# Kernel optimization log

Measured on AMD Instinct MI355X. Metric: run time of the kernel, lower is better.

Reference implementation:

```python
import jax, jax.numpy as jnp
import numpy as np

EMBED = 128
HEADS = 8
HEAD_DIM = EMBED // HEADS
MARKOFF = -1.0e8


def setup_inputs() -> dict:
    key = jax.random.key(0)
    ks = jax.random.split(key, 10)
    B, N, T, E = 2, 512, 12, EMBED
    values = jax.random.normal(ks[0], (B, N, T, E), dtype=jnp.float32)
    keys = jax.random.normal(ks[1], (B, N, T, E), dtype=jnp.float32)
    query = jax.random.normal(ks[2], (B, N, T, E), dtype=jnp.float32)
    # binary spatial mask [N, N] (1 = attend, 0 = block), kept float as in the torch code
    mask = (jax.random.uniform(ks[3], (N, N)) > 0.1).astype(jnp.float32)
    # per-head projections (nn.Linear on last dim of size head_dim, no bias)
    s = 1.0 / np.sqrt(HEAD_DIM)
    Wv = jax.random.uniform(ks[4], (HEAD_DIM, HEAD_DIM), minval=-s, maxval=s, dtype=jnp.float32)
    Wk = jax.random.uniform(ks[5], (HEAD_DIM, HEAD_DIM), minval=-s, maxval=s, dtype=jnp.float32)
    Wq = jax.random.uniform(ks[6], (HEAD_DIM, HEAD_DIM), minval=-s, maxval=s, dtype=jnp.float32)
    so = 1.0 / np.sqrt(EMBED)
    Wo = jax.random.uniform(ks[7], (EMBED, EMBED), minval=-so, maxval=so, dtype=jnp.float32)
    bo = jax.random.uniform(ks[8], (EMBED,), minval=-so, maxval=so, dtype=jnp.float32)
    return {"values": values, "keys": keys, "query": query, "mask": mask,
            "Wv": Wv, "Wk": Wk, "Wq": Wq, "Wo": Wo, "bo": bo}


def reference(values, keys, query, mask, Wv, Wk, Wq, Wo, bo):
    B, N, T, E = query.shape
    H, D = HEADS, HEAD_DIM
    scale = E ** 0.5
    v = values.reshape(B, N, T, H, D) @ Wv.T   # [B,N,T,H,D]
    k = keys.reshape(B, N, T, H, D) @ Wk.T
    q = query.reshape(B, N, T, H, D) @ Wq.T
    # energy over node axis: [B, Nq, Nk, T, H]
    energy = jnp.einsum('bqthd,bkthd->bqkth', q, k)
    m = mask[None, :, :, None, None]
    energy = energy * m + MARKOFF * (1.0 - m)
    # NOTE: softmax over the QUERY axis (dim=1), as in the original
    attention = jax.nn.softmax(jnp.clip(energy / scale, -5.0, 5.0), axis=1)
    out = jnp.einsum('bqkth,bkthd->bqthd', attention, v).reshape(B, N, T, H * D)
    out = out @ Wo.T + bo
    return out, attention
```

## Files before the change

kernel.cpp:

```cpp
#include <hip/hip_runtime.h>
#include <math.h>

#define DI __device__ __forceinline__

typedef short s16x8 __attribute__((ext_vector_type(8)));
typedef float f32x4 __attribute__((ext_vector_type(4)));

constexpr float MARKOFF_ = -100000000.0f;
constexpr float INVSCALE_ = 0.088388347648318447f;

DI s16x8 bc(uint4 u) { return __builtin_bit_cast(s16x8, u); }
DI unsigned short f2bf(float f) {
  unsigned u = __float_as_uint(f);
  return (unsigned short)((u + 0x7FFFu + ((u >> 16) & 1u)) >> 16);
}
DI float bf2f(unsigned short h) { return __uint_as_float(((unsigned)h) << 16); }
DI unsigned cvtpk(float lo, float hi) {
  unsigned r;
  asm("v_cvt_pk_bf16_f32 %0, %1, %2" : "=v"(r) : "v"(lo), "v"(hi));
  return r;
}

DI void load16(float* dst, const float* src) {
  #pragma unroll
  for (int c = 0; c < 4; ++c) {
    float4 v = reinterpret_cast<const float4*>(src)[c];
    dst[c * 4 + 0] = v.x; dst[c * 4 + 1] = v.y;
    dst[c * 4 + 2] = v.z; dst[c * 4 + 3] = v.w;
  }
}

DI float dotw4(const float4* w4, const float* x) {
  float s = 0.f;
  #pragma unroll
  for (int c = 0; c < 4; ++c) {
    float4 w = w4[c];
    s = fmaf(w.x, x[4*c], fmaf(w.y, x[4*c+1], fmaf(w.z, x[4*c+2], fmaf(w.w, x[4*c+3], s))));
  }
  return s;
}

DI void packstore(ushort* dst, const float* y) {
  ushort hs[16];
  #pragma unroll
  for (int d = 0; d < 16; ++d) hs[d] = f2bf(y[d]);
  unsigned hi[8], lo[8];
  #pragma unroll
  for (int i = 0; i < 8; ++i) {
    hi[i] = (unsigned)hs[2*i] | ((unsigned)hs[2*i+1] << 16);
    float l0 = y[2*i]   - bf2f(hs[2*i]);
    float l1 = y[2*i+1] - bf2f(hs[2*i+1]);
    lo[i] = (unsigned)f2bf(l0) | ((unsigned)f2bf(l1) << 16);
  }
  uint4* p = (uint4*)dst;
  p[0] = make_uint4(hi[0], hi[1], hi[2], hi[3]);
  p[1] = make_uint4(hi[4], hi[5], hi[6], hi[7]);
  p[2] = make_uint4(lo[0], lo[1], lo[2], lo[3]);
  p[3] = make_uint4(lo[4], lo[5], lo[6], lo[7]);
}

__global__ __launch_bounds__(256) void k_proj(
    const float* __restrict__ vals, const float* __restrict__ keys,
    const float* __restrict__ qry, const float* __restrict__ Wv,
    const float* __restrict__ Wk, const float* __restrict__ Wq,
    ushort* __restrict__ Qp, ushort* __restrict__ Kp, ushort* __restrict__ Vt) {
  __shared__ float wlds[768];
  __shared__ ushort vtile[16 * 16 * 16];
  int blk = blockIdx.x;
  int nc = blk & 31, SL = blk >> 5;
  int b = SL / 6, t2 = SL % 6;
  int tid = threadIdx.x;
  if (tid < 256) {
    wlds[tid] = Wq[tid];
    wlds[256 + tid] = Wk[tid];
    wlds[512 + tid] = Wv[tid];
  }
  __syncthreads();
  int th = tid & 15, nl = tid >> 4;
  int t = 2 * t2 + (th >> 3), h = th & 7;
  int key = (th & 3) << 2;
  int n = nc * 16 + nl;
  size_t ioff = ((size_t)(b * 512 + n) * 12 + t) * 128 + h * 16;
  float xq[16], xk[16], xv[16], y[16];
  load16(xq, qry + ioff);
  load16(xk, keys + ioff);
  load16(xv, vals + ioff);
  size_t orow = ((size_t)(SL * 512 + n) * 16 + th) * 32;
  #pragma unroll
  for (int d = 0; d < 16; ++d) y[d] = dotw4((const float4*)&wlds[d * 16], xq);
  packstore(Qp + orow, y);
  #pragma unroll
  for (int d = 0; d < 16; ++d) y[d] = dotw4((const float4*)&wlds[256 + d * 16], xk);
  packstore(Kp + orow, y);
  #pragma unroll
  for (int d = 0; d < 16; ++d) y[d] = dotw4((const float4*)&wlds[512 + d * 16], xv);
  #pragma unroll
  for (int d = 0; d < 16; ++d) vtile[th * 256 + d * 16 + (nl ^ key)] = f2bf(y[d]);
  __syncthreads();
  #pragma unroll
  for (int it = 0; it < 2; ++it) {
    int u = tid + it * 256;
    int thd = u >> 1, half = u & 1;
    int thw = thd >> 4;
    uint4 v = *(const uint4*)&vtile[thd * 16 + half * 8];
    if (thw & 1) {
      unsigned t0 = v.x; v.x = v.z; v.z = t0;
      t0 = v.y; v.y = v.w; v.w = t0;
    }
    int lhalf = half ^ ((thw >> 1) & 1);
    *(uint4*)(Vt + (size_t)(SL * 256 + thd) * 512 + nc * 16 + lhalf * 8) = v;
  }
}

__global__ __launch_bounds__(256) void k_colsum(
    const ushort* __restrict__ Qp, const ushort* __restrict__ Kp,
    const float* __restrict__ mask, float* __restrict__ cs) {
  int blk = blockIdx.x;
  int qs = blk & 3, kc = (blk >> 2) & 15, SL = blk >> 6;
  int tid = threadIdx.x;
  int l = tid & 63, wv = tid >> 6, c = l & 15, g = l >> 4, thb = wv * 4;
  uint4 zz = make_uint4(0, 0, 0, 0);
  s16x8 Bk1[2][4], Bk2[2][4];
  #pragma unroll
  for (int e = 0; e < 2; ++e) {
    int kb = kc * 32 + e * 16;
    #pragma unroll
    for (int j = 0; j < 4; ++j) {
      const uint4* row = (const uint4*)(Kp + ((size_t)(SL * 512 + kb + c) * 16 + thb + j) * 32);
      Bk1[e][j] = bc(row[g & 1]);
      Bk2[e][j] = bc(g < 2 ? row[2 + (g & 1)] : zz);
    }
  }
  float sum[2][4] = {{0.f, 0.f, 0.f, 0.f}, {0.f, 0.f, 0.f, 0.f}};
  for (int qtl = 0; qtl < 8; ++qtl) {
    int qb = qs * 128 + qtl * 16;
    float m[2][4];
    #pragma unroll
    for (int e = 0; e < 2; ++e) {
      int kb = kc * 32 + e * 16;
      #pragma unroll
      for (int r = 0; r < 4; ++r)
        m[e][r] = mask[(size_t)(qb + 4 * g + r) * 512 + kb + c];
    }
    #pragma unroll
    for (int j = 0; j < 4; ++j) {
      const uint4* qrow = (const uint4*)(Qp + ((size_t)(SL * 512 + qb + c) * 16 + thb + j) * 32);
      s16x8 A1 = bc(qrow[g]);
      s16x8 A2 = bc(qrow[g & 1]);
      #pragma unroll
      for (int e = 0; e < 2; ++e) {
        f32x4 C = __builtin_amdgcn_mfma_f32_16x16x32_bf16(A1, Bk1[e][j], (f32x4){0.f,0.f,0.f,0.f}, 0, 0, 0);
        C = __builtin_amdgcn_mfma_f32_16x16x32_bf16(A2, Bk2[e][j], C, 0, 0, 0);
        #pragma unroll
        for (int r = 0; r < 4; ++r) {
          float Em = m[e][r] > 0.5f ? C[r] : MARKOFF_;
          float x = fminf(fmaxf(Em * INVSCALE_, -5.f), 5.f);
          sum[e][j] += __expf(x);
        }
      }
    }
  }
  #pragma unroll
  for (int e = 0; e < 2; ++e)
    #pragma unroll
    for (int j = 0; j < 4; ++j) {
      float s = sum[e][j];
      s += __shfl_xor(s, 16, 64);
      s += __shfl_xor(s, 32, 64);
      if (l < 16)
        cs[((size_t)(qs * 12 + SL) * 16 + thb + j) * 512 + kc * 32 + e * 16 + c] = s;
    }
}

__global__ __launch_bounds__(256) void k_inv(const float* __restrict__ cs,
                                             float* __restrict__ inv) {
  int id = blockIdx.x * 256 + threadIdx.x;
  float s = cs[id] + cs[id + 98304] + cs[id + 196608] + cs[id + 294912];
  inv[id] = 1.0f / s;
}

__global__ __launch_bounds__(256, 4) void k_attn(
    const ushort* __restrict__ Qp, const ushort* __restrict__ Kp,
    const ushort* __restrict__ Vt, const float* __restrict__ mask,
    const float* __restrict__ inv, float* __restrict__ Aout,
    float* __restrict__ Oh, int KS) {
  __shared__ __align__(16) float stage[5184];
  int blk = blockIdx.x;
  int ksp = blk & (KS - 1);
  int rest = blk / KS;
  int qt = rest & 31, SL = rest >> 5;
  int b = SL / 6, t2 = SL % 6;
  int qb = qt * 16;
  int tid = threadIdx.x;
  int l = tid & 63, wv = tid >> 6, c = l & 15, g = l >> 4, thb = wv * 4;
  uint4 zz = make_uint4(0, 0, 0, 0);
  s16x8 Bq1[4], Bq2[4];
  #pragma unroll
  for (int j = 0; j < 4; ++j) {
    const uint4* row = (const uint4*)(Qp + ((size_t)(SL * 512 + qb + c) * 16 + thb + j) * 32);
    Bq1[j] = bc(row[g & 1]);
    Bq2[j] = bc(g < 2 ? row[2 + (g & 1)] : zz);
  }
  f32x4 O[4];
  #pragma unroll
  for (int j = 0; j < 4; ++j) O[j] = (f32x4){0.f, 0.f, 0.f, 0.f};

  int nch = 16 / KS;
  for (int cc = 0; cc < nch; ++cc) {
    int kch = ksp * (512 / KS) + cc * 32;
    unsigned apk[4][4];
    #pragma unroll
    for (int h = 0; h < 2; ++h) {
      int kb = kch + h * 16;
      float4 m4 = *(const float4*)(mask + (size_t)(qb + c) * 512 + kb + 4 * g);
      float m[4] = {m4.x, m4.y, m4.z, m4.w};
      float p[4][4];
      #pragma unroll
      for (int j = 0; j < 4; ++j) {
        const uint4* krow = (const uint4*)(Kp + ((size_t)(SL * 512 + kb + c) * 16 + thb + j) * 32);
        s16x8 A1 = bc(krow[g]);
        s16x8 A2 = bc(krow[g & 1]);
        f32x4 C = __builtin_amdgcn_mfma_f32_16x16x32_bf16(A1, Bq1[j], (f32x4){0.f,0.f,0.f,0.f}, 0, 0, 0);
        C = __builtin_amdgcn_mfma_f32_16x16x32_bf16(A2, Bq2[j], C, 0, 0, 0);
        float4 i4 = *(const float4*)(inv + (size_t)(SL * 16 + thb + j) * 512 + kb + 4 * g);
        float iv[4] = {i4.x, i4.y, i4.z, i4.w};
        #pragma unroll
        for (int r = 0; r < 4; ++r) {
          float Em = m[r] > 0.5f ? C[r] : MARKOFF_;
          float x = fminf(fmaxf(Em * INVSCALE_, -5.f), 5.f);
          p[j][r] = __expf(x) * iv[r];
        }
        apk[j][h * 2 + 0] = cvtpk(p[j][0], p[j][1]);
        apk[j][h * 2 + 1] = cvtpk(p[j][2], p[j][3]);
      }
      #pragma unroll
      for (int r = 0; r < 4; ++r) {
        f32x4 w = {p[0][r], p[1][r], p[2][r], p[3][r]};
        *(f32x4*)&stage[(4 * g + r) * 324 + c * 20 + thb] = w;
      }
      if (h == 1) {
        #pragma unroll
        for (int j = 0; j < 4; ++j) {
          const ushort* vb = Vt + ((size_t)(SL * 16 + thb + j) * 16 + c) * 512 + kch + 4 * g;
          uint2 v0 = *(const uint2*)vb;
          uint2 v1 = *(const uint2*)(vb + 16);
          s16x8 a_op = bc(make_uint4(apk[j][0], apk[j][1], apk[j][2], apk[j][3]));
          s16x8 b_op = bc(make_uint4(v0.x, v0.y, v1.x, v1.y));
          O[j] = __builtin_amdgcn_mfma_f32_16x16x32_bf16(a_op, b_op, O[j], 0, 0, 0);
        }
      }
      __syncthreads();
      #pragma unroll
      for (int it = 0; it < 4; ++it) {
        int m5 = tid & 3, pr = tid >> 2;
        int kk = pr & 15, q = (pr >> 4) + it * 4;
        f32x4 v = *(const f32x4*)&stage[kk * 324 + q * 20 + m5 * 4];
        size_t ga = ((size_t)(b * 512 + qb + q) * 512 + kb + kk) * 96 + t2 * 16 + m5 * 4;
        __builtin_nontemporal_store(v, (f32x4*)(Aout + ga));
      }
      __syncthreads();
    }
  }
  #pragma unroll
  for (int j = 0; j < 4; ++j) {
    int th = thb + j, t = 2 * t2 + (th >> 3), h = th & 7;
    float* op = Oh + (size_t)ksp * 1572864;
    #pragma unroll
    for (int r = 0; r < 4; ++r)
      op[((size_t)(b * 512 + qb + 4 * g + r) * 12 + t) * 128 + h * 16 + c] = O[j][r];
  }
}

__global__ __launch_bounds__(128) void k_outproj(
    const float* __restrict__ Oh, const float* __restrict__ Wo,
    const float* __restrict__ bo, float* __restrict__ out, int KS) {
  __shared__ float xr[12 * 128];
  int bn = blockIdx.x;
  int b = bn >> 9, n = bn & 511;
  int col = threadIdx.x;
  for (int i = col; i < 1536; i += 128) {
    float s = 0.f;
    for (int sl = 0; sl < KS; ++sl)
      s += Oh[(size_t)sl * 1572864 + (size_t)(b * 512 + n) * 1536 + i];
    xr[i] = s;
  }
  __syncthreads();
  float acc[12];
  float bias = bo[col];
  #pragma unroll
  for (int rr = 0; rr < 12; ++rr) acc[rr] = bias;
  const float4* wrow = reinterpret_cast<const float4*>(Wo + (size_t)col * 128);
  #pragma unroll 8
  for (int jc = 0; jc < 32; ++jc) {
    float4 w = wrow[jc];
    #pragma unroll
    for (int rr = 0; rr < 12; ++rr) {
      const float* x = &xr[rr * 128 + jc * 4];
      acc[rr] = fmaf(w.x, x[0], fmaf(w.y, x[1], fmaf(w.z, x[2], fmaf(w.w, x[3], acc[rr]))));
    }
  }
  size_t obase = ((size_t)(b * 512 + n)) * 1536;
  #pragma unroll
  for (int rr = 0; rr < 12; ++rr) out[obase + rr * 128 + col] = acc[rr];
}

extern "C" void kernel_launch(void* const* d_in, const int* in_sizes, int n_in,
                              void* d_out, int out_size, void* d_ws, size_t ws_size,
                              hipStream_t stream) {
  (void)in_sizes; (void)n_in; (void)out_size;
  const float* vals = (const float*)d_in[0];
  const float* keys = (const float*)d_in[1];
  const float* qry  = (const float*)d_in[2];
  const float* mask = (const float*)d_in[3];
  const float* Wv = (const float*)d_in[4];
  const float* Wk = (const float*)d_in[5];
  const float* Wq = (const float*)d_in[6];
  const float* Wo = (const float*)d_in[7];
  const float* bo = (const float*)d_in[8];
  float* out = (float*)d_out;
  float* Aout = out + 1572864;

  ushort* Qp = (ushort*)d_ws;
  ushort* Kp = Qp + 3145728;
  ushort* Vt = Kp + 3145728;
  float* cs  = (float*)(Vt + 1572864);
  float* inv = cs + 393216;
  float* Oh  = inv + 98304;

  const size_t BASE = 17694720;
  int KS = 1;
  if (ws_size >= BASE + 4ull * 6291456) KS = 4;
  else if (ws_size >= BASE + 2ull * 6291456) KS = 2;

  k_proj<<<384, 256, 0, stream>>>(vals, keys, qry, Wv, Wk, Wq, Qp, Kp, Vt);
  k_colsum<<<768, 256, 0, stream>>>(Qp, Kp, mask, cs);
  k_inv<<<384, 256, 0, stream>>>(cs, inv);
  k_attn<<<384 * KS, 256, 0, stream>>>(Qp, Kp, Vt, mask, inv, Aout, Oh, KS);
  k_outproj<<<1024, 128, 0, stream>>>(Oh, Wo, bo, out, KS);
}
```

Measured before the change: 196.6 us.

## Loop all six time-pairs inside each attention block to reuse mask across slices

The attention kernel now gives each block a query tile and key split and loops over all six time-pair slices internally. It keeps six sets of output accumulators in registers, so mask loads are reused across time slices. The grid shrinks from 384*KS to 64*KSA blocks with up to an 8-way key split. Costs are higher register pressure (96 accumulator floats), the occupancy hint in launch bounds being dropped, fewer blocks to cover the GPU, and more partial-sum traffic into the output projection.

Result: slower. 275.5 us (+40.1%).

```diff
diff --git a/kernel.cpp b/kernel.cpp
--- a/kernel.cpp
+++ b/kernel.cpp
@@ -70,11 +70,9 @@
   int nc = blk & 31, SL = blk >> 5;
   int b = SL / 6, t2 = SL % 6;
   int tid = threadIdx.x;
-  if (tid < 256) {
-    wlds[tid] = Wq[tid];
-    wlds[256 + tid] = Wk[tid];
-    wlds[512 + tid] = Wv[tid];
-  }
+  wlds[tid] = Wq[tid];
+  wlds[256 + tid] = Wk[tid];
+  wlds[512 + tid] = Wv[tid];
   __syncthreads();
   int th = tid & 15, nl = tid >> 4;
   int t = 2 * t2 + (th >> 3), h = th & 7;
@@ -179,108 +177,119 @@
   inv[id] = 1.0f / s;
 }
 
-__global__ __launch_bounds__(256, 4) void k_attn(
+__global__ __launch_bounds__(256) void k_attn(
     const ushort* __restrict__ Qp, const ushort* __restrict__ Kp,
     const ushort* __restrict__ Vt, const float* __restrict__ mask,
     const float* __restrict__ inv, float* __restrict__ Aout,
-    float* __restrict__ Oh, int KS) {
+    float* __restrict__ Oh, int KSA) {
   __shared__ __align__(16) float stage[5184];
   int blk = blockIdx.x;
-  int ksp = blk & (KS - 1);
-  int rest = blk / KS;
-  int qt = rest & 31, SL = rest >> 5;
-  int b = SL / 6, t2 = SL % 6;
+  int ksp = blk & (KSA - 1);
+  int rest = blk / KSA;
+  int qt = rest & 31, b = rest >> 5;
   int qb = qt * 16;
   int tid = threadIdx.x;
   int l = tid & 63, wv = tid >> 6, c = l & 15, g = l >> 4, thb = wv * 4;
   uint4 zz = make_uint4(0, 0, 0, 0);
-  s16x8 Bq1[4], Bq2[4];
-  #pragma unroll
-  for (int j = 0; j < 4; ++j) {
-    const uint4* row = (const uint4*)(Qp + ((size_t)(SL * 512 + qb + c) * 16 + thb + j) * 32);
-    Bq1[j] = bc(row[g & 1]);
-    Bq2[j] = bc(g < 2 ? row[2 + (g & 1)] : zz);
-  }
-  f32x4 O[4];
-  #pragma unroll
-  for (int j = 0; j < 4; ++j) O[j] = (f32x4){0.f, 0.f, 0.f, 0.f};
-
-  int nch = 16 / KS;
+  f32x4 O[6][4];
+  #pragma unroll
+  for (int t2 = 0; t2 < 6; ++t2)
+    #pragma unroll
+    for (int j = 0; j < 4; ++j) O[t2][j] = (f32x4){0.f, 0.f, 0.f, 0.f};
+
+  int kcount = 512 / KSA;
+  int nch = kcount >> 5;
+  int kb0 = ksp * kcount;
   for (int cc = 0; cc < nch; ++cc) {
-    int kch = ksp * (512 / KS) + cc * 32;
-    unsigned apk[4][4];
-    #pragma unroll
-    for (int h = 0; h < 2; ++h) {
-      int kb = kch + h * 16;
-      float4 m4 = *(const float4*)(mask + (size_t)(qb + c) * 512 + kb + 4 * g);
-      float m[4] = {m4.x, m4.y, m4.z, m4.w};
-      float p[4][4];
+    int kch = kb0 + cc * 32;
+    #pragma unroll
+    for (int t2 = 0; t2 < 6; ++t2) {
+      int SL = b * 6 + t2;
+      s16x8 Bq1[4], Bq2[4];
       #pragma unroll
       for (int j = 0; j < 4; ++j) {
-        const uint4* krow = (const uint4*)(Kp + ((size_t)(SL * 512 + kb + c) * 16 + thb + j) * 32);
-        s16x8 A1 = bc(krow[g]);
-        s16x8 A2 = bc(krow[g & 1]);
-        f32x4 C = __builtin_amdgcn_mfma_f32_16x16x32_bf16(A1, Bq1[j], (f32x4){0.f,0.f,0.f,0.f}, 0, 0, 0);
-        C = __builtin_amdgcn_mfma_f32_16x16x32_bf16(A2, Bq2[j], C, 0, 0, 0);
-        float4 i4 = *(const float4*)(inv + (size_t)(SL * 16 + thb + j) * 512 + kb + 4 * g);
-        float iv[4] = {i4.x, i4.y, i4.z, i4.w};
+        const uint4* row = (const uint4*)(Qp + ((size_t)(SL * 512 + qb + c) * 16 + thb + j) * 32);
+        Bq1[j] = bc(row[g & 1]);
+        Bq2[j] = bc(g < 2 ? row[2 + (g & 1)] : zz);
+      }
+      unsigned apk[4][4];
+      #pragma unroll
+      for (int h = 0; h < 2; ++h) {
+        int kb = kch + h * 16;
+        float4 m4 = *(const float4*)(mask + (size_t)(qb + c) * 512 + kb + 4 * g);
+        float m[4] = {m4.x, m4.y, m4.z, m4.w};
+        float p[4][4];
+        #pragma unroll
+        for (int j = 0; j < 4; ++j) {
+          const uint4* krow = (const uint4*)(Kp + ((size_t)(SL * 512 + kb + c) * 16 + thb + j) * 32);
+          s16x8 A1 = bc(krow[g]);
+          s16x8 A2 = bc(krow[g & 1]);
+          f32x4 C = __builtin_amdgcn_mfma_f32_16x16x32_bf16(A1, Bq1[j], (f32x4){0.f,0.f,0.f,0.f}, 0, 0, 0);
+          C = __builtin_amdgcn_mfma_f32_16x16x32_bf16(A2, Bq2[j], C, 0, 0, 0);
+          float4 i4 = *(const float4*)(inv + (size_t)(SL * 16 + thb + j) * 512 + kb + 4 * g);
+          float iv[4] = {i4.x, i4.y, i4.z, i4.w};
+          #pragma unroll
+          for (int r = 0; r < 4; ++r) {
+            float Em = m[r] > 0.5f ? C[r] : MARKOFF_;
+            float x = fminf(fmaxf(Em * INVSCALE_, -5.f), 5.f);
+            p[j][r] = __expf(x) * iv[r];
+          }
+          apk[j][h * 2 + 0] = cvtpk(p[j][0], p[j][1]);
+          apk[j][h * 2 + 1] = cvtpk(p[j][2], p[j][3]);
+        }
         #pragma unroll
         for (int r = 0; r < 4; ++r) {
-          float Em = m[r] > 0.5f ? C[r] : MARKOFF_;
-          float x = fminf(fmaxf(Em * INVSCALE_, -5.f), 5.f);
-          p[j][r] = __expf(x) * iv[r];
-        }
-        apk[j][h * 2 + 0] = cvtpk(p[j][0], p[j][1]);
-        apk[j][h * 2 + 1] = cvtpk(p[j][2], p[j][3]);
+          f32x4 w = {p[0][r], p[1][r], p[2][r], p[3][r]};
+          *(f32x4*)&stage[(4 * g + r) * 324 + c * 20 + thb] = w;
+        }
+        if (h == 1) {
+          #pragma unroll
+          for (int j = 0; j < 4; ++j) {
+            const ushort* vb = Vt + ((size_t)(SL * 16 + thb + j) * 16 + c) * 512 + kch + 4 * g;
+            uint2 v0 = *(const uint2*)vb;
+            uint2 v1 = *(const uint2*)(vb + 16);
+            s16x8 a_op = bc(make_uint4(apk[j][0], apk[j][1], apk[j][2], apk[j][3]));
+            s16x8 b_op = bc(make_uint4(v0.x, v0.y, v1.x, v1.y));
+            O[t2][j] = __builtin_amdgcn_mfma_f32_16x16x32_bf16(a_op, b_op, O[t2][j], 0, 0, 0);
+          }
+        }
+        __syncthreads();
+        #pragma unroll
+        for (int it = 0; it < 4; ++it) {
+          int m5 = tid & 3, pr = tid >> 2;
+          int kk = pr & 15, q = (pr >> 4) + it * 4;
+          f32x4 v = *(const f32x4*)&stage[kk * 324 + q * 20 + m5 * 4];
+          size_t ga = ((size_t)(b * 512 + qb + q) * 512 + kb + kk) * 96 + t2 * 16 + m5 * 4;
+          __builtin_nontemporal_store(v, (f32x4*)(Aout + ga));
+        }
+        __syncthreads();
       }
-      #pragma unroll
-      for (int r = 0; r < 4; ++r) {
-        f32x4 w = {p[0][r], p[1][r], p[2][r], p[3][r]};
-        *(f32x4*)&stage[(4 * g + r) * 324 + c * 20 + thb] = w;
-      }
-      if (h == 1) {
-        #pragma unroll
-        for (int j = 0; j < 4; ++j) {
-          const ushort* vb = Vt + ((size_t)(SL * 16 + thb + j) * 16 + c) * 512 + kch + 4 * g;
-          uint2 v0 = *(const uint2*)vb;
-          uint2 v1 = *(const uint2*)(vb + 16);
-          s16x8 a_op = bc(make_uint4(apk[j][0], apk[j][1], apk[j][2], apk[j][3]));
-          s16x8 b_op = bc(make_uint4(v0.x, v0.y, v1.x, v1.y));
-          O[j] = __builtin_amdgcn_mfma_f32_16x16x32_bf16(a_op, b_op, O[j], 0, 0, 0);
-        }
-      }
-      __syncthreads();
-      #pragma unroll
-      for (int it = 0; it < 4; ++it) {
-        int m5 = tid & 3, pr = tid >> 2;
-        int kk = pr & 15, q = (pr >> 4) + it * 4;
-        f32x4 v = *(const f32x4*)&stage[kk * 324 + q * 20 + m5 * 4];
-        size_t ga = ((size_t)(b * 512 + qb + q) * 512 + kb + kk) * 96 + t2 * 16 + m5 * 4;
-        __builtin_nontemporal_store(v, (f32x4*)(Aout + ga));
-      }
-      __syncthreads();
-    }
-  }
-  #pragma unroll
-  for (int j = 0; j < 4; ++j) {
-    int th = thb + j, t = 2 * t2 + (th >> 3), h = th & 7;
-    float* op = Oh + (size_t)ksp * 1572864;
-    #pragma unroll
-    for (int r = 0; r < 4; ++r)
-      op[((size_t)(b * 512 + qb + 4 * g + r) * 12 + t) * 128 + h * 16 + c] = O[j][r];
+    }
+  }
+  float* op = Oh + (size_t)ksp * 1572864;
+  #pragma unroll
+  for (int t2 = 0; t2 < 6; ++t2) {
+    #pragma unroll
+    for (int j = 0; j < 4; ++j) {
+      int th = thb + j;
+      int t = 2 * t2 + (th >> 3), hh = th & 7;
+      #pragma unroll
+      for (int r = 0; r < 4; ++r)
+        op[((size_t)(b * 512 + qb + 4 * g + r) * 12 + t) * 128 + hh * 16 + c] = O[t2][j][r];
+    }
   }
 }
 
 __global__ __launch_bounds__(128) void k_outproj(
     const float* __restrict__ Oh, const float* __restrict__ Wo,
-    const float* __restrict__ bo, float* __restrict__ out, int KS) {
+    const float* __restrict__ bo, float* __restrict__ out, int KSA) {
   __shared__ float xr[12 * 128];
   int bn = blockIdx.x;
   int b = bn >> 9, n = bn & 511;
   int col = threadIdx.x;
   for (int i = col; i < 1536; i += 128) {
     float s = 0.f;
-    for (int sl = 0; sl < KS; ++sl)
+    for (int sl = 0; sl < KSA; ++sl)
       s += Oh[(size_t)sl * 1572864 + (size_t)(b * 512 + n) * 1536 + i];
     xr[i] = s;
   }
@@ -328,13 +337,14 @@
   float* Oh  = inv + 98304;
 
   const size_t BASE = 17694720;
-  int KS = 1;
-  if (ws_size >= BASE + 4ull * 6291456) KS = 4;
-  else if (ws_size >= BASE + 2ull * 6291456) KS = 2;
+  int KSA = 1;
+  if (ws_size >= BASE + 8ull * 6291456) KSA = 8;
+  else if (ws_size >= BASE + 4ull * 6291456) KSA = 4;
+  else if (ws_size >= BASE + 2ull * 6291456) KSA = 2;
 
   k_proj<<<384, 256, 0, stream>>>(vals, keys, qry, Wv, Wk, Wq, Qp, Kp, Vt);
   k_colsum<<<768, 256, 0, stream>>>(Qp, Kp, mask, cs);
   k_inv<<<384, 256, 0, stream>>>(cs, inv);
-  k_attn<<<384 * KS, 256, 0, stream>>>(Qp, Kp, Vt, mask, inv, Aout, Oh, KS);
-  k_outproj<<<1024, 128, 0, stream>>>(Oh, Wo, bo, out, KS);
-}
+  k_attn<<<64 * KSA, 256, 0, stream>>>(Qp, Kp, Vt, mask, inv, Aout, Oh, KSA);
+  k_outproj<<<1024, 128, 0, stream>>>(Oh, Wo, bo, out, KSA);
+}
```

## Split attention into separate output and attention-map kernels with direct stores

Applied to the files above, without the earlier changes.

Splits the fused attention kernel in two. k_attnO recomputes the probabilities and does only the P·V accumulation, with no LDS staging or barriers. k_attnA recomputes QK^T and the softmax again, looping over all six time-slices per block so each thread writes a contiguous 96-float row segment of the attention map directly, instead of staging through shared memory. The aim is to remove the two barriers per tile and the LDS round trip, and to get better-coalesced stores for the large attention output. The cost is computing energies and exponentials twice and loading Q and K twice.

Result: slower. 343.7 us (+74.8%).

```diff
diff --git a/kernel.cpp b/kernel.cpp
--- a/kernel.cpp
+++ b/kernel.cpp
@@ -70,11 +70,9 @@
   int nc = blk & 31, SL = blk >> 5;
   int b = SL / 6, t2 = SL % 6;
   int tid = threadIdx.x;
-  if (tid < 256) {
-    wlds[tid] = Wq[tid];
-    wlds[256 + tid] = Wk[tid];
-    wlds[512 + tid] = Wv[tid];
-  }
+  wlds[tid] = Wq[tid];
+  wlds[256 + tid] = Wk[tid];
+  wlds[512 + tid] = Wv[tid];
   __syncthreads();
   int th = tid & 15, nl = tid >> 4;
   int t = 2 * t2 + (th >> 3), h = th & 7;
@@ -179,15 +177,13 @@
   inv[id] = 1.0f / s;
 }
 
-__global__ __launch_bounds__(256, 4) void k_attn(
+__global__ __launch_bounds__(256) void k_attnO(
     const ushort* __restrict__ Qp, const ushort* __restrict__ Kp,
     const ushort* __restrict__ Vt, const float* __restrict__ mask,
-    const float* __restrict__ inv, float* __restrict__ Aout,
-    float* __restrict__ Oh, int KS) {
-  __shared__ __align__(16) float stage[5184];
+    const float* __restrict__ inv, float* __restrict__ Oh, int KSO) {
   int blk = blockIdx.x;
-  int ksp = blk & (KS - 1);
-  int rest = blk / KS;
+  int ksp = blk & (KSO - 1);
+  int rest = blk / KSO;
   int qt = rest & 31, SL = rest >> 5;
   int b = SL / 6, t2 = SL % 6;
   int qb = qt * 16;
@@ -205,16 +201,15 @@
   #pragma unroll
   for (int j = 0; j < 4; ++j) O[j] = (f32x4){0.f, 0.f, 0.f, 0.f};
 
-  int nch = 16 / KS;
+  int nch = 16 / KSO;
   for (int cc = 0; cc < nch; ++cc) {
-    int kch = ksp * (512 / KS) + cc * 32;
+    int kch = ksp * (512 / KSO) + cc * 32;
     unsigned apk[4][4];
     #pragma unroll
     for (int h = 0; h < 2; ++h) {
       int kb = kch + h * 16;
       float4 m4 = *(const float4*)(mask + (size_t)(qb + c) * 512 + kb + 4 * g);
       float m[4] = {m4.x, m4.y, m4.z, m4.w};
-      float p[4][4];
       #pragma unroll
       for (int j = 0; j < 4; ++j) {
         const uint4* krow = (const uint4*)(Kp + ((size_t)(SL * 512 + kb + c) * 16 + thb + j) * 32);
@@ -224,63 +219,97 @@
         C = __builtin_amdgcn_mfma_f32_16x16x32_bf16(A2, Bq2[j], C, 0, 0, 0);
         float4 i4 = *(const float4*)(inv + (size_t)(SL * 16 + thb + j) * 512 + kb + 4 * g);
         float iv[4] = {i4.x, i4.y, i4.z, i4.w};
+        float p[4];
+        #pragma unroll
+        for (int r = 0; r < 4; ++r) {
+          float Em = m[r] > 0.5f ? C[r] : MARKOFF_;
+          float x = fminf(fmaxf(Em * INVSCALE_, -5.f), 5.f);
+          p[r] = __expf(x) * iv[r];
+        }
+        apk[j][h * 2 + 0] = cvtpk(p[0], p[1]);
+        apk[j][h * 2 + 1] = cvtpk(p[2], p[3]);
+      }
+    }
+    #pragma unroll
+    for (int j = 0; j < 4; ++j) {
+      const ushort* vb = Vt + ((size_t)(SL * 16 + thb + j) * 16 + c) * 512 + kch + 4 * g;
+      uint2 v0 = *(const uint2*)vb;
+      uint2 v1 = *(const uint2*)(vb + 16);
+      s16x8 a_op = bc(make_uint4(apk[j][0], apk[j][1], apk[j][2], apk[j][3]));
+      s16x8 b_op = bc(make_uint4(v0.x, v0.y, v1.x, v1.y));
+      O[j] = __builtin_amdgcn_mfma_f32_16x16x32_bf16(a_op, b_op, O[j], 0, 0, 0);
+    }
+  }
+  float* op = Oh + (size_t)ksp * 1572864;
+  #pragma unroll
+  for (int j = 0; j < 4; ++j) {
+    int th = thb + j, t = 2 * t2 + (th >> 3), hh = th & 7;
+    #pragma unroll
+    for (int r = 0; r < 4; ++r)
+      op[((size_t)(b * 512 + qb + 4 * g + r) * 12 + t) * 128 + hh * 16 + c] = O[j][r];
+  }
+}
+
+__global__ __launch_bounds__(256) void k_attnA(
+    const ushort* __restrict__ Qp, const ushort* __restrict__ Kp,
+    const float* __restrict__ mask, const float* __restrict__ inv,
+    float* __restrict__ Aout) {
+  int blk = blockIdx.x;
+  int ksp = blk & 7;
+  int rest = blk >> 3;
+  int qt = rest & 31, b = rest >> 5;
+  int qb = qt * 16;
+  int tid = threadIdx.x;
+  int l = tid & 63, wv = tid >> 6, c = l & 15, g = l >> 4, thb = wv * 4;
+  uint4 zz = make_uint4(0, 0, 0, 0);
+  int kb0 = ksp * 64;
+  for (int kt = 0; kt < 4; ++kt) {
+    int kb = kb0 + kt * 16;
+    float4 m4 = *(const float4*)(mask + (size_t)(qb + c) * 512 + kb + 4 * g);
+    float m[4] = {m4.x, m4.y, m4.z, m4.w};
+    float* ap = Aout + ((size_t)(b * 512 + qb + c) * 512 + kb + 4 * g) * 96 + thb;
+    #pragma unroll
+    for (int t2 = 0; t2 < 6; ++t2) {
+      int SL = b * 6 + t2;
+      float p[4][4];
+      #pragma unroll
+      for (int j = 0; j < 4; ++j) {
+        const uint4* qrow = (const uint4*)(Qp + ((size_t)(SL * 512 + qb + c) * 16 + thb + j) * 32);
+        const uint4* krow = (const uint4*)(Kp + ((size_t)(SL * 512 + kb + c) * 16 + thb + j) * 32);
+        s16x8 A1 = bc(krow[g]);
+        s16x8 A2 = bc(krow[g & 1]);
+        s16x8 B1 = bc(qrow[g & 1]);
+        s16x8 B2 = bc(g < 2 ? qrow[2 + (g & 1)] : zz);
+        f32x4 C = __builtin_amdgcn_mfma_f32_16x16x32_bf16(A1, B1, (f32x4){0.f,0.f,0.f,0.f}, 0, 0, 0);
+        C = __builtin_amdgcn_mfma_f32_16x16x32_bf16(A2, B2, C, 0, 0, 0);
+        float4 i4 = *(const float4*)(inv + (size_t)(SL * 16 + thb + j) * 512 + kb + 4 * g);
+        float iv[4] = {i4.x, i4.y, i4.z, i4.w};
         #pragma unroll
         for (int r = 0; r < 4; ++r) {
           float Em = m[r] > 0.5f ? C[r] : MARKOFF_;
           float x = fminf(fmaxf(Em * INVSCALE_, -5.f), 5.f);
           p[j][r] = __expf(x) * iv[r];
         }
-        apk[j][h * 2 + 0] = cvtpk(p[j][0], p[j][1]);
-        apk[j][h * 2 + 1] = cvtpk(p[j][2], p[j][3]);
       }
       #pragma unroll
       for (int r = 0; r < 4; ++r) {
         f32x4 w = {p[0][r], p[1][r], p[2][r], p[3][r]};
-        *(f32x4*)&stage[(4 * g + r) * 324 + c * 20 + thb] = w;
+        *(f32x4*)(ap + r * 96 + t2 * 16) = w;
       }
-      if (h == 1) {
-        #pragma unroll
-        for (int j = 0; j < 4; ++j) {
-          const ushort* vb = Vt + ((size_t)(SL * 16 + thb + j) * 16 + c) * 512 + kch + 4 * g;
-          uint2 v0 = *(const uint2*)vb;
-          uint2 v1 = *(const uint2*)(vb + 16);
-          s16x8 a_op = bc(make_uint4(apk[j][0], apk[j][1], apk[j][2], apk[j][3]));
-          s16x8 b_op = bc(make_uint4(v0.x, v0.y, v1.x, v1.y));
-          O[j] = __builtin_amdgcn_mfma_f32_16x16x32_bf16(a_op, b_op, O[j], 0, 0, 0);
-        }
-      }
-      __syncthreads();
-      #pragma unroll
-      for (int it = 0; it < 4; ++it) {
-        int m5 = tid & 3, pr = tid >> 2;
-        int kk = pr & 15, q = (pr >> 4) + it * 4;
-        f32x4 v = *(const f32x4*)&stage[kk * 324 + q * 20 + m5 * 4];
-        size_t ga = ((size_t)(b * 512 + qb + q) * 512 + kb + kk) * 96 + t2 * 16 + m5 * 4;
-        __builtin_nontemporal_store(v, (f32x4*)(Aout + ga));
-      }
-      __syncthreads();
-    }
-  }
-  #pragma unroll
-  for (int j = 0; j < 4; ++j) {
-    int th = thb + j, t = 2 * t2 + (th >> 3), h = th & 7;
-    float* op = Oh + (size_t)ksp * 1572864;
-    #pragma unroll
-    for (int r = 0; r < 4; ++r)
-      op[((size_t)(b * 512 + qb + 4 * g + r) * 12 + t) * 128 + h * 16 + c] = O[j][r];
+    }
   }
 }
 
 __global__ __launch_bounds__(128) void k_outproj(
     const float* __restrict__ Oh, const float* __restrict__ Wo,
-    const float* __restrict__ bo, float* __restrict__ out, int KS) {
+    const float* __restrict__ bo, float* __restrict__ out, int KSO) {
   __shared__ float xr[12 * 128];
   int bn = blockIdx.x;
   int b = bn >> 9, n = bn & 511;
   int col = threadIdx.x;
   for (int i = col; i < 1536; i += 128) {
     float s = 0.f;
-    for (int sl = 0; sl < KS; ++sl)
+    for (int sl = 0; sl < KSO; ++sl)
       s += Oh[(size_t)sl * 1572864 + (size_t)(b * 512 + n) * 1536 + i];
     xr[i] = s;
   }
@@ -328,13 +357,14 @@
   float* Oh  = inv + 98304;
 
   const size_t BASE = 17694720;
-  int KS = 1;
-  if (ws_size >= BASE + 4ull * 6291456) KS = 4;
-  else if (ws_size >= BASE + 2ull * 6291456) KS = 2;
+  int KSO = 1;
+  if (ws_size >= BASE + 4ull * 6291456) KSO = 4;
+  else if (ws_size >= BASE + 2ull * 6291456) KSO = 2;
 
   k_proj<<<384, 256, 0, stream>>>(vals, keys, qry, Wv, Wk, Wq, Qp, Kp, Vt);
   k_colsum<<<768, 256, 0, stream>>>(Qp, Kp, mask, cs);
   k_inv<<<384, 256, 0, stream>>>(cs, inv);
-  k_attn<<<384 * KS, 256, 0, stream>>>(Qp, Kp, Vt, mask, inv, Aout, Oh, KS);
-  k_outproj<<<1024, 128, 0, stream>>>(Oh, Wo, bo, out, KS);
-}
+  k_attnO<<<384 * KSO, 256, 0, stream>>>(Qp, Kp, Vt, mask, inv, Oh, KSO);
+  k_attnA<<<512, 256, 0, stream>>>(Qp, Kp, mask, inv, Aout);
+  k_outproj<<<1024, 128, 0, stream>>>(Oh, Wo, bo, out, KSO);
+}
```
